# Kernel tuning notes

Hardware: AMD Instinct MI355X
Metric: run time of the kernel (lower is better)

The kernel has to match this reference:

```python
import jax, jax.numpy as jnp
import numpy as np

IN_DIM = 8192
OUT_DIM = 4096
NNZ = 1638400
BATCH = 4096


def setup_inputs() -> dict:
    key = jax.random.key(0)
    k_x, k_r, k_c, k_w = jax.random.split(key, 4)
    x = jax.random.normal(k_x, (BATCH, IN_DIM), dtype=jnp.float32)
    row_idx = jax.random.randint(k_r, (NNZ,), 0, IN_DIM, dtype=jnp.int64)
    col_idx = jax.random.randint(k_c, (NNZ,), 0, OUT_DIM, dtype=jnp.int64)
    # xavier_uniform on a [nnz, 1] tensor: bound = sqrt(6 / (nnz + 1))
    bound = float(np.sqrt(6.0 / (NNZ + 1)))
    weights = jax.random.uniform(k_w, (NNZ,), dtype=jnp.float32, minval=-bound, maxval=bound)
    bias = jnp.zeros((OUT_DIM,), dtype=jnp.float32)
    return {"x": x, "row_idx": row_idx, "col_idx": col_idx, "weights": weights, "bias": bias}


def reference(x, row_idx, col_idx, weights, bias):
    # scatter_nd: build dense [IN_DIM, OUT_DIM] weight matrix via scatter-add
    ind1d = row_idx * OUT_DIM + col_idx  # flat indices, duplicates accumulate
    W = jnp.zeros((IN_DIM * OUT_DIM,), dtype=weights.dtype).at[ind1d].add(weights)
    W = W.reshape(IN_DIM, OUT_DIM)
    # dense matmul + bias, matching torch.mm(x, sparse_tensor) + bias
    return x @ W + bias
```

## Files before the change

kernel.cpp:

```cpp
#include <hip/hip_runtime.h>
#include <hip/hip_bf16.h>
#include <stdint.h>

#define IN_DIM 8192
#define OUT_DIM 4096
#define NNZ 1638400
#define BATCH 4096

#define BM 128
#define BN 128
#define BK 64

typedef __bf16 bf16x8 __attribute__((ext_vector_type(8)));
typedef float f32x4 __attribute__((ext_vector_type(4)));


__device__ __forceinline__ unsigned short f2bf(float f) {
  union { float f; unsigned int u; } v; v.f = f;
  unsigned int u = v.u;
  unsigned int r = (u + 0x7FFFu + ((u >> 16) & 1u)) >> 16;
  return (unsigned short)r;
}

__device__ __forceinline__ float bf2f(unsigned short b) {
  union { unsigned int u; float f; } v;
  v.u = (unsigned int)b << 16;
  return v.f;
}

__device__ __forceinline__ void async16(const void* g, void* l) {
  __builtin_amdgcn_global_load_lds(
      (const __attribute__((address_space(1))) unsigned int*)g,
      (__attribute__((address_space(3))) unsigned int*)l,
      16, 0, 0);
}

__device__ __forceinline__ void convert_body(int i, const float* __restrict__ src,
                                             unsigned short* __restrict__ dst) {
  const float4* s = (const float4*)src;
  float4 a = s[2 * i];
  float4 b = s[2 * i + 1];
  union { unsigned short us[8]; uint4 v; } o;
  o.us[0] = f2bf(a.x); o.us[1] = f2bf(a.y); o.us[2] = f2bf(a.z); o.us[3] = f2bf(a.w);
  o.us[4] = f2bf(b.x); o.us[5] = f2bf(b.y); o.us[6] = f2bf(b.z); o.us[7] = f2bf(b.w);
  ((uint4*)dst)[i] = o.v;
}


#define PREP_BLOCKS ((IN_DIM * OUT_DIM) / 8 / 256)

__global__ void prep_kernel(uint4* __restrict__ W_zero,
                            const float* __restrict__ x,
                            unsigned short* __restrict__ x_bf16) {
  int i = blockIdx.x * 256 + threadIdx.x;
  W_zero[i] = make_uint4(0, 0, 0, 0);
  convert_body(i, x, x_bf16);
}


__device__ __forceinline__ void scat1(int c, int r, float w,
                                      unsigned int* __restrict__ W) {
  size_t e = (size_t)c * IN_DIM + r;
  unsigned int* p = W + (e >> 1);
  const bool hi = (e & 1);
  unsigned int cur = *p;
  unsigned int assumed;
  do {
    assumed = cur;
    unsigned short h = hi ? (unsigned short)(assumed >> 16)
                          : (unsigned short)(assumed & 0xFFFFu);
    unsigned short nb = f2bf(bf2f(h) + w);
    unsigned int nw = hi ? ((assumed & 0x0000FFFFu) | ((unsigned int)nb << 16))
                         : ((assumed & 0xFFFF0000u) | (unsigned int)nb);
    cur = atomicCAS(p, assumed, nw);
  } while (cur != assumed);
}

#define SCAT_BLOCKS (NNZ / 4 / 256)

__global__ void scatter_kernel(const int4* __restrict__ ri4,
                               const int4* __restrict__ ci4,
                               const float4* __restrict__ w4,
                               unsigned int* __restrict__ W) {
  int i = blockIdx.x * 256 + threadIdx.x;
  int4 r = ri4[i];
  int4 c = ci4[i];
  float4 w = w4[i];
  scat1(c.x, r.x, w.x, W);
  scat1(c.y, r.y, w.y, W);
  scat1(c.z, r.z, w.z, W);
  scat1(c.w, r.w, w.w, W);
}


__global__ __launch_bounds__(256) void gemm_kernel(
    const unsigned short* __restrict__ A,
    const unsigned short* __restrict__ Bt,
    const float* __restrict__ bias,
    float* __restrict__ C) {
  __shared__ alignas(16) unsigned short lA[BM * BK];
  __shared__ alignas(16) unsigned short lB[BN * BK];

  const int tid = threadIdx.x;
  const int m0 = blockIdx.y * BM;
  const int n0 = blockIdx.x * BN;

  const int wid = tid >> 6;
  const int lane = tid & 63;
  const int wm = wid >> 1;
  const int wn = wid & 1;
  const int quad = lane >> 4;
  const int lm = lane & 15;
  const int xorv = lm & 7;

  f32x4 acc[4][4] = {};

  int srow[4], sgs[4];
#pragma unroll
  for (int c = 0; c < 4; ++c) {
    int t2 = c * 256 + tid;
    srow[c] = t2 >> 3;
    sgs[c] = (t2 & 7) ^ (srow[c] & 7);
  }

  for (int kt = 0; kt < IN_DIM / BK; ++kt) {
    const int k0 = kt * BK;
#pragma unroll
    for (int c = 0; c < 4; ++c) {
      const int t2 = c * 256 + tid;
      async16(A + (size_t)(m0 + srow[c]) * IN_DIM + k0 + sgs[c] * 8,
              (char*)lA + t2 * 16);
      async16(Bt + (size_t)(n0 + srow[c]) * IN_DIM + k0 + sgs[c] * 8,
              (char*)lB + t2 * 16);
    }

    __syncthreads();

#pragma unroll
    for (int s = 0; s < 2; ++s) {
      bf16x8 af[4], bfr[4];
#pragma unroll
      for (int i = 0; i < 4; ++i) {
        const int row = wm * 64 + i * 16 + lm;
        const int p = ((s << 2) | quad) ^ xorv;
        af[i] = *(const bf16x8*)(lA + row * BK + p * 8);
      }
#pragma unroll
      for (int j = 0; j < 4; ++j) {
        const int row = wn * 64 + j * 16 + lm;
        const int p = ((s << 2) | quad) ^ xorv;
        bfr[j] = *(const bf16x8*)(lB + row * BK + p * 8);
      }
#pragma unroll
      for (int i = 0; i < 4; ++i)
#pragma unroll
        for (int j = 0; j < 4; ++j)
          acc[i][j] = __builtin_amdgcn_mfma_f32_16x16x32_bf16(af[i], bfr[j], acc[i][j], 0, 0, 0);
    }

    __syncthreads();
  }

  const int ccol0 = n0 + wn * 64 + lm;
  const int crow0 = m0 + wm * 64;
#pragma unroll
  for (int j = 0; j < 4; ++j) {
    const int col = ccol0 + j * 16;
    const float bv = bias[col];
#pragma unroll
    for (int i = 0; i < 4; ++i) {
#pragma unroll
      for (int v = 0; v < 4; ++v) {
        const int row = crow0 + i * 16 + quad * 4 + v;
        C[(size_t)row * OUT_DIM + col] = acc[i][j][v] + bv;
      }
    }
  }
}


extern "C" void kernel_launch(void* const* d_in, const int* in_sizes, int n_in,
                              void* d_out, int out_size, void* d_ws, size_t ws_size,
                              hipStream_t stream) {
  const float* x = (const float*)d_in[0];
  const int* row_idx = (const int*)d_in[1];
  const int* col_idx = (const int*)d_in[2];
  const float* weights = (const float*)d_in[3];
  const float* bias = (const float*)d_in[4];
  float* out = (float*)d_out;

  const size_t W_BF16_BYTES = (size_t)IN_DIM * OUT_DIM * 2;
  unsigned short* W_bf16 = (unsigned short*)d_ws;
  unsigned short* x_bf16 = (unsigned short*)((char*)d_ws + W_BF16_BYTES);

  prep_kernel<<<PREP_BLOCKS, 256, 0, stream>>>((uint4*)W_bf16, x, x_bf16);

  scatter_kernel<<<SCAT_BLOCKS, 256, 0, stream>>>(
      (const int4*)row_idx, (const int4*)col_idx, (const float4*)weights,
      (unsigned int*)W_bf16);

  dim3 grid(OUT_DIM / BN, BATCH / BM);
  gemm_kernel<<<grid, 256, 0, stream>>>(x_bf16, W_bf16, bias, out);
}
```

Measured before the change: 595.1 us.

## Use 256x256 double-buffered GEMM tiles and packed bf16 atomic scatter

The GEMM moves to 256x256 tiles with 512 threads and double-buffered LDS (128 KB dynamic), prefetching the next K tile in stages while issuing MFMAs with raised priority. Blocks are also remapped with an XOR swizzle to improve L2 locality. The scatter replaces the CAS loop with a hardware packed bf16 atomic add when the builtin is available, or else tries a single CAS against zero first. The new code relies on 128 KB of LDS per block, a larger register footprint, and hardware bf16 atomic rounding.

```diff
diff --git a/kernel.cpp b/kernel.cpp
--- a/kernel.cpp
+++ b/kernel.cpp
@@ -1,5 +1,4 @@
 #include <hip/hip_runtime.h>
-#include <hip/hip_bf16.h>
 #include <stdint.h>
 
 #define IN_DIM 8192
@@ -7,12 +6,9 @@
 #define NNZ 1638400
 #define BATCH 4096
 
-#define BM 128
-#define BN 128
-#define BK 64
-
 typedef __bf16 bf16x8 __attribute__((ext_vector_type(8)));
 typedef float f32x4 __attribute__((ext_vector_type(4)));
+typedef short s16x2 __attribute__((ext_vector_type(2)));
 
 
 __device__ __forceinline__ unsigned short f2bf(float f) {
@@ -58,22 +54,39 @@
 }
 
 
+#if defined(__has_builtin)
+#  if __has_builtin(__builtin_amdgcn_global_atomic_fadd_v2bf16)
+#    define HAVE_PK_BF16 1
+#  endif
+#endif
+
 __device__ __forceinline__ void scat1(int c, int r, float w,
                                       unsigned int* __restrict__ W) {
   size_t e = (size_t)c * IN_DIM + r;
+  const bool hi = (e & 1);
+  unsigned short nb = f2bf(w);
+#ifdef HAVE_PK_BF16
+  s16x2 v;
+  v.x = hi ? (short)0 : (short)nb;
+  v.y = hi ? (short)nb : (short)0;
+  __builtin_amdgcn_global_atomic_fadd_v2bf16(
+      (__attribute__((address_space(1))) s16x2*)(W + (e >> 1)), v);
+#else
   unsigned int* p = W + (e >> 1);
-  const bool hi = (e & 1);
-  unsigned int cur = *p;
+  unsigned int nw0 = hi ? ((unsigned int)nb << 16) : (unsigned int)nb;
+  unsigned int cur = atomicCAS(p, 0u, nw0);
+  if (cur == 0u) return;
   unsigned int assumed;
   do {
     assumed = cur;
     unsigned short h = hi ? (unsigned short)(assumed >> 16)
                           : (unsigned short)(assumed & 0xFFFFu);
-    unsigned short nb = f2bf(bf2f(h) + w);
-    unsigned int nw = hi ? ((assumed & 0x0000FFFFu) | ((unsigned int)nb << 16))
-                         : ((assumed & 0xFFFF0000u) | (unsigned int)nb);
+    unsigned short b2 = f2bf(bf2f(h) + w);
+    unsigned int nw = hi ? ((assumed & 0x0000FFFFu) | ((unsigned int)b2 << 16))
+                         : ((assumed & 0xFFFF0000u) | (unsigned int)b2);
     cur = atomicCAS(p, assumed, nw);
   } while (cur != assumed);
+#endif
 }
 
 #define SCAT_BLOCKS (NNZ / 4 / 256)
@@ -93,82 +106,120 @@
 }
 
 
-__global__ __launch_bounds__(256) void gemm_kernel(
+#define TBM 256
+#define TBN 256
+#define TBK 64
+#define NKT (IN_DIM / TBK)
+
+__global__ __launch_bounds__(512, 2) void gemm_kernel(
     const unsigned short* __restrict__ A,
     const unsigned short* __restrict__ Bt,
     const float* __restrict__ bias,
     float* __restrict__ C) {
-  __shared__ alignas(16) unsigned short lA[BM * BK];
-  __shared__ alignas(16) unsigned short lB[BN * BK];
+  extern __shared__ __align__(16) unsigned short lds[];
 
   const int tid = threadIdx.x;
-  const int m0 = blockIdx.y * BM;
-  const int n0 = blockIdx.x * BN;
+
+  const int bid = blockIdx.x;
+  const int swz = ((bid & 7) << 5) | (bid >> 3);
+  const int m0 = (swz & 15) * TBM;
+  const int n0 = (swz >> 4) * TBN;
 
   const int wid = tid >> 6;
   const int lane = tid & 63;
-  const int wm = wid >> 1;
-  const int wn = wid & 1;
+  const int wm = wid >> 2;
+  const int wn = wid & 3;
   const int quad = lane >> 4;
   const int lm = lane & 15;
   const int xorv = lm & 7;
 
-  f32x4 acc[4][4] = {};
-
-  int srow[4], sgs[4];
+  const unsigned short* Ab = A + (size_t)m0 * IN_DIM;
+  const unsigned short* Bb = Bt + (size_t)n0 * IN_DIM;
+
+  int soff[4], ldst[4];
 #pragma unroll
   for (int c = 0; c < 4; ++c) {
-    int t2 = c * 256 + tid;
-    srow[c] = t2 >> 3;
-    sgs[c] = (t2 & 7) ^ (srow[c] & 7);
-  }
-
-  for (int kt = 0; kt < IN_DIM / BK; ++kt) {
-    const int k0 = kt * BK;
-#pragma unroll
-    for (int c = 0; c < 4; ++c) {
-      const int t2 = c * 256 + tid;
-      async16(A + (size_t)(m0 + srow[c]) * IN_DIM + k0 + sgs[c] * 8,
-              (char*)lA + t2 * 16);
-      async16(Bt + (size_t)(n0 + srow[c]) * IN_DIM + k0 + sgs[c] * 8,
-              (char*)lB + t2 * 16);
+    const int t2 = c * 512 + tid;
+    const int srow = t2 >> 3;
+    const int sseg = (t2 & 7) ^ (srow & 7);
+    soff[c] = srow * IN_DIM + sseg * 8;
+    ldst[c] = t2 * 16;
+  }
+
+  f32x4 acc[8][4] = {};
+
+#define STAGE(kt_, b_, c_)                                                  \
+  do {                                                                      \
+    const int k0_ = (kt_)*TBK;                                              \
+    char* la_ = (char*)lds + (b_)*65536;                                    \
+    async16(Ab + (size_t)soff[c_] + k0_, la_ + ldst[c_]);                   \
+    async16(Bb + (size_t)soff[c_] + k0_, la_ + 32768 + ldst[c_]);           \
+  } while (0)
+
+#pragma unroll
+  for (int c = 0; c < 4; ++c) STAGE(0, 0, c);
+
+  for (int kt = 0; kt < NKT; ++kt) {
+    const int buf = kt & 1;
+    const int nbuf = buf ^ 1;
+    const int ktn = (kt + 1) & (NKT - 1);
+
+    STAGE(ktn, nbuf, 0);
+    asm volatile("s_waitcnt vmcnt(2)" ::: "memory");
+    __builtin_amdgcn_sched_barrier(0);
+    __builtin_amdgcn_s_barrier();
+
+    const unsigned short* lA = lds + buf * 32768;
+    const unsigned short* lB = lA + 16384;
+
+    bf16x8 bfr[4][2];
+#pragma unroll
+    for (int j = 0; j < 4; ++j) {
+      const int row = wn * 64 + j * 16 + lm;
+#pragma unroll
+      for (int ss = 0; ss < 2; ++ss) {
+        const int p = ((ss << 2) | quad) ^ xorv;
+        bfr[j][ss] = *(const bf16x8*)(lB + row * TBK + p * 8);
+      }
     }
 
-    __syncthreads();
-
-#pragma unroll
-    for (int s = 0; s < 2; ++s) {
-      bf16x8 af[4], bfr[4];
-#pragma unroll
-      for (int i = 0; i < 4; ++i) {
-        const int row = wm * 64 + i * 16 + lm;
-        const int p = ((s << 2) | quad) ^ xorv;
-        af[i] = *(const bf16x8*)(lA + row * BK + p * 8);
+#pragma unroll
+    for (int q = 0; q < 4; ++q) {
+      bf16x8 af[2][2];
+#pragma unroll
+      for (int i = 0; i < 2; ++i) {
+        const int row = wm * 128 + (q * 2 + i) * 16 + lm;
+#pragma unroll
+        for (int ss = 0; ss < 2; ++ss) {
+          const int p = ((ss << 2) | quad) ^ xorv;
+          af[i][ss] = *(const bf16x8*)(lA + row * TBK + p * 8);
+        }
       }
-#pragma unroll
-      for (int j = 0; j < 4; ++j) {
-        const int row = wn * 64 + j * 16 + lm;
-        const int p = ((s << 2) | quad) ^ xorv;
-        bfr[j] = *(const bf16x8*)(lB + row * BK + p * 8);
-      }
-#pragma unroll
-      for (int i = 0; i < 4; ++i)
+      if (q < 3) STAGE(ktn, nbuf, q + 1);
+      __builtin_amdgcn_s_barrier();
+      __builtin_amdgcn_s_setprio(1);
+#pragma unroll
+      for (int i = 0; i < 2; ++i)
 #pragma unroll
         for (int j = 0; j < 4; ++j)
-          acc[i][j] = __builtin_amdgcn_mfma_f32_16x16x32_bf16(af[i], bfr[j], acc[i][j], 0, 0, 0);
+#pragma unroll
+          for (int ss = 0; ss < 2; ++ss)
+            acc[q * 2 + i][j] = __builtin_amdgcn_mfma_f32_16x16x32_bf16(
+                af[i][ss], bfr[j][ss], acc[q * 2 + i][j], 0, 0, 0);
+      __builtin_amdgcn_s_setprio(0);
+      __builtin_amdgcn_s_barrier();
     }
-
-    __syncthreads();
-  }
+  }
+#undef STAGE
 
   const int ccol0 = n0 + wn * 64 + lm;
-  const int crow0 = m0 + wm * 64;
+  const int crow0 = m0 + wm * 128;
 #pragma unroll
   for (int j = 0; j < 4; ++j) {
     const int col = ccol0 + j * 16;
     const float bv = bias[col];
 #pragma unroll
-    for (int i = 0; i < 4; ++i) {
+    for (int i = 0; i < 8; ++i) {
 #pragma unroll
       for (int v = 0; v < 4; ++v) {
         const int row = crow0 + i * 16 + quad * 4 + v;
@@ -193,12 +244,19 @@
   unsigned short* W_bf16 = (unsigned short*)d_ws;
   unsigned short* x_bf16 = (unsigned short*)((char*)d_ws + W_BF16_BYTES);
 
+  static bool attr_set = false;
+  if (!attr_set) {
+    (void)hipFuncSetAttribute((const void*)gemm_kernel,
+                              hipFuncAttributeMaxDynamicSharedMemorySize,
+                              131072);
+    attr_set = true;
+  }
+
   prep_kernel<<<PREP_BLOCKS, 256, 0, stream>>>((uint4*)W_bf16, x, x_bf16);
 
   scatter_kernel<<<SCAT_BLOCKS, 256, 0, stream>>>(
       (const int4*)row_idx, (const int4*)col_idx, (const float4*)weights,
       (unsigned int*)W_bf16);
 
-  dim3 grid(OUT_DIM / BN, BATCH / BM);
-  gemm_kernel<<<grid, 256, 0, stream>>>(x_bf16, W_bf16, bias, out);
-}
+  gemm_kernel<<<dim3(256), dim3(512), 131072, stream>>>(x_bf16, W_bf16, bias, out);
+}
```

New measurement: 522.8 us. 12.2% less time.
